# Performance work log

Measured on AMD Instinct MI355X. Metric: run time of the kernel, lower is better.

The kernel has to match this reference:

```python
import jax, jax.numpy as jnp
import numpy as np


def setup_inputs() -> dict:
    key = jax.random.key(0)
    k1, k2, k3 = jax.random.split(key, 3)
    B, C, H, W = 4, 320, 135, 240
    pnum = int(540 * 960 * 0.025)  # 12960, from shape=(540,960), sparse_rate=0.025
    x = jax.random.normal(k1, (B, C, H, W), dtype=jnp.float32)
    unc = jax.random.uniform(k2, (H, W), dtype=jnp.float32)
    prompts = jax.random.normal(k3, (pnum, C, 1, 1), dtype=jnp.float32)
    return {"x": x, "unc": unc, "prompts": prompts}


def reference(x, unc, prompts):
    # x: (B, C=320, H, W) bottleneck feature map; unc: (H, W); prompts: (pnum, C, 1, 1)
    H, W = x.shape[2], x.shape[3]
    pnum = prompts.shape[0]
    # descending top-k over flattened uncertainty map (== argsort()[::-1][:pnum])
    _, topk = jax.lax.top_k(unc.reshape(-1), pnum)  # (pnum,)
    hs = topk // W
    ws = topk % W
    # bilinear interpolation of a 1x1 spatial map is a pure broadcast, so
    # resized_prompt[j, :, 0, 0] == prompts[j, :, 0, 0]
    pv = prompts[:, :, 0, 0]  # (pnum, C)
    # scatter-add prompt vector j into feat[:, :, hs[j], ws[j]] across batch
    return x.at[:, :, hs, ws].add(pv.T[None])  # (B, C, H, W)
```

## Files before the change

### kernel.cpp

```cpp
#include <hip/hip_runtime.h>
#include <stdint.h>

#define BB    4
#define CC    320
#define HH    135
#define WW    240
#define HW    (HH*WW)
#define PNUM  12960
#define NBUCK 16384
#define MAXPER 32
#define P4    (HW/4)
#define NCH   4
#define NTILE ((CC/NCH)*P4)

typedef float f4 __attribute__((ext_vector_type(4)));
typedef unsigned u4 __attribute__((ext_vector_type(4)));

__global__ __launch_bounds__(256) void k_bucket(const float* __restrict__ unc,
                                                unsigned* __restrict__ hist,
                                                unsigned* __restrict__ members) {
    int i = blockIdx.x * 256 + threadIdx.x;
    if (i >= HW) return;
    float v = unc[i];
    int b = (int)(v * (float)NBUCK);
    b = b < 0 ? 0 : (b > NBUCK - 1 ? NBUCK - 1 : b);
    unsigned pos = atomicAdd(&hist[b], 1u);
    if (pos < MAXPER) members[(unsigned)b * MAXPER + pos] = (unsigned)i;
}

__global__ __launch_bounds__(1024) void k_scan(const unsigned* __restrict__ hist,
                                               unsigned* __restrict__ base) {
    __shared__ unsigned sh[1024];
    const int CH = NBUCK / 1024;
    int t = threadIdx.x;
    unsigned loc[CH];
    unsigned s = 0;
    #pragma unroll
    for (int k = 0; k < CH; ++k) { loc[k] = hist[t * CH + k]; s += loc[k]; }
    sh[t] = s;
    __syncthreads();
    for (int off = 1; off < 1024; off <<= 1) {
        unsigned v = (t + off < 1024) ? sh[t + off] : 0u;
        __syncthreads();
        sh[t] += v;
        __syncthreads();
    }
    unsigned run = sh[t] - s;
    #pragma unroll
    for (int k = CH - 1; k >= 0; --k) { base[t * CH + k] = run; run += loc[k]; }
}

__global__ __launch_bounds__(256) void k_rank(const float* __restrict__ unc,
                                              const unsigned* __restrict__ hist,
                                              const unsigned* __restrict__ base,
                                              const unsigned* __restrict__ members,
                                              unsigned* __restrict__ rank) {
    int i = blockIdx.x * 256 + threadIdx.x;
    if (i >= HW) return;
    float vi = unc[i];
    int b = (int)(vi * (float)NBUCK);
    b = b < 0 ? 0 : (b > NBUCK - 1 ? NBUCK - 1 : b);
    unsigned cnt = hist[b];
    if (cnt > MAXPER) cnt = MAXPER;
    unsigned r = base[b];
    for (unsigned k = 0; k < cnt; ++k) {
        unsigned j = members[(unsigned)b * MAXPER + k];
        if (j == (unsigned)i) continue;
        float vj = unc[j];
        r += (vj > vi) || (vj == vi && j < (unsigned)i);
    }
    rank[i] = r;
}

__global__ __launch_bounds__(256) void k_apply(const float* __restrict__ x,
                                               const float* __restrict__ prompts,
                                               const unsigned* __restrict__ rank,
                                               float* __restrict__ out) {
    int t = blockIdx.x * 256 + threadIdx.x;
    if (t >= NTILE) return;
    int cg = t / P4;
    int p4 = t - cg * P4;
    int c0 = cg * NCH;
    int p  = p4 * 4;

    u4 r4 = *(const u4*)(rank + p);

    float g[4][NCH];
    #pragma unroll
    for (int k = 0; k < 4; ++k) {
        unsigned r = r4[k];
        f4 gv = (f4)(0.0f);
        if (r < PNUM) gv = *(const f4*)(prompts + (size_t)r * CC + c0);
        #pragma unroll
        for (int j = 0; j < NCH; ++j) g[k][j] = gv[j];
    }

    #pragma unroll
    for (int b = 0; b < BB; ++b) {
        #pragma unroll
        for (int j = 0; j < NCH; ++j) {
            int off = (b * CC + c0 + j) * HW + p;
            f4 xv = __builtin_nontemporal_load((const f4*)(x + off));
            xv[0] += g[0][j]; xv[1] += g[1][j]; xv[2] += g[2][j]; xv[3] += g[3][j];
            __builtin_nontemporal_store(xv, (f4*)(out + off));
        }
    }
}

extern "C" void kernel_launch(void* const* d_in, const int* in_sizes, int n_in,
                              void* d_out, int out_size, void* d_ws, size_t ws_size,
                              hipStream_t stream) {
    const float* x       = (const float*)d_in[0];
    const float* unc     = (const float*)d_in[1];
    const float* prompts = (const float*)d_in[2];
    float* out = (float*)d_out;

    char* ws = (char*)d_ws;
    unsigned* hist    = (unsigned*)(ws);
    unsigned* base    = (unsigned*)(ws + (size_t)NBUCK * 4);
    unsigned* members = (unsigned*)(ws + (size_t)NBUCK * 8);
    unsigned* rank    = (unsigned*)(ws + (size_t)NBUCK * 8 + (size_t)NBUCK * MAXPER * 4);

    hipMemsetAsync(hist, 0, (size_t)NBUCK * 4, stream);
    k_bucket<<<(HW + 255) / 256, 256, 0, stream>>>(unc, hist, members);
    k_scan<<<1, 1024, 0, stream>>>(hist, base);
    k_rank<<<(HW + 255) / 256, 256, 0, stream>>>(unc, hist, base, members, rank);
    k_apply<<<(NTILE + 255) / 256, 256, 0, stream>>>(x, prompts, rank, out);
}
```

Before: 88.80 us.

## Precompute dense bf16 prompt-delta buffer and apply with contiguous loads

Adds a gather pass that writes a dense per-pixel, per-channel-group delta buffer in bf16, so the apply kernel reads contiguous vectors instead of doing random prompt gathers per tile. It also replaces hipMemsetAsync with a small zeroing kernel and drops the nontemporal load and store hints in the new apply path. The cost is an extra kernel launch and roughly 20 MB of extra memory traffic, and the bf16 rounding of the prompt values adds numerical error. The fallback path runs only when the workspace is too small.

Result: slower. 106.1 us (+19.4%).

```diff
diff --git a/kernel.cpp b/kernel.cpp
--- a/kernel.cpp
+++ b/kernel.cpp
@@ -11,10 +11,21 @@
 #define MAXPER 32
 #define P4    (HW/4)
 #define NCH   4
-#define NTILE ((CC/NCH)*P4)
+#define NCG   (CC/NCH)
+#define NTILE (NCG*P4)
 
 typedef float f4 __attribute__((ext_vector_type(4)));
 typedef unsigned u4 __attribute__((ext_vector_type(4)));
+
+__device__ inline unsigned short f2bf(float x) {
+    unsigned u = __float_as_uint(x);
+    return (unsigned short)((u + 0x7fffu + ((u >> 16) & 1u)) >> 16);
+}
+
+__global__ __launch_bounds__(256) void k_zero(unsigned* __restrict__ hist) {
+    int i = blockIdx.x * 256 + threadIdx.x;
+    if (i < NBUCK) hist[i] = 0u;
+}
 
 __global__ __launch_bounds__(256) void k_bucket(const float* __restrict__ unc,
                                                 unsigned* __restrict__ hist,
@@ -72,10 +83,25 @@
     rank[i] = r;
 }
 
-__global__ __launch_bounds__(256) void k_apply(const float* __restrict__ x,
-                                               const float* __restrict__ prompts,
-                                               const unsigned* __restrict__ rank,
-                                               float* __restrict__ out) {
+__global__ __launch_bounds__(256) void k_gather(const float* __restrict__ prompts,
+                                                const unsigned* __restrict__ rank,
+                                                unsigned* __restrict__ dbuf) {
+    int t = blockIdx.x * 256 + threadIdx.x;
+    if (t >= NCG * HW) return;
+    int cg = t / HW;
+    int p  = t - cg * HW;
+    unsigned r = rank[p];
+    f4 gv = (f4)(0.0f);
+    if (r < PNUM) gv = *(const f4*)(prompts + (size_t)r * CC + cg * 4);
+    uint2 w;
+    w.x = (unsigned)f2bf(gv[0]) | ((unsigned)f2bf(gv[1]) << 16);
+    w.y = (unsigned)f2bf(gv[2]) | ((unsigned)f2bf(gv[3]) << 16);
+    *(uint2*)(dbuf + 2 * (size_t)t) = w;
+}
+
+__global__ __launch_bounds__(256) void k_apply2(const float* __restrict__ x,
+                                                const unsigned* __restrict__ dbuf,
+                                                float* __restrict__ out) {
     int t = blockIdx.x * 256 + threadIdx.x;
     if (t >= NTILE) return;
     int cg = t / P4;
@@ -83,8 +109,45 @@
     int c0 = cg * NCH;
     int p  = p4 * 4;
 
+    const unsigned* dp = dbuf + 2 * ((size_t)cg * HW + p);
+    u4 A  = *(const u4*)dp;
+    u4 Bv = *(const u4*)(dp + 4);
+
+    float g[4][4];
+    #pragma unroll
+    for (int k = 0; k < 4; ++k) {
+        unsigned w0 = (k < 2) ? A[2 * k]     : Bv[2 * k - 4];
+        unsigned w1 = (k < 2) ? A[2 * k + 1] : Bv[2 * k - 3];
+        g[k][0] = __uint_as_float(w0 << 16);
+        g[k][1] = __uint_as_float(w0 & 0xffff0000u);
+        g[k][2] = __uint_as_float(w1 << 16);
+        g[k][3] = __uint_as_float(w1 & 0xffff0000u);
+    }
+
+    #pragma unroll
+    for (int b = 0; b < BB; ++b) {
+        #pragma unroll
+        for (int j = 0; j < NCH; ++j) {
+            int off = (b * CC + c0 + j) * HW + p;
+            f4 xv = *(const f4*)(x + off);
+            xv[0] += g[0][j]; xv[1] += g[1][j]; xv[2] += g[2][j]; xv[3] += g[3][j];
+            *(f4*)(out + off) = xv;
+        }
+    }
+}
+
+#define OFFS(it) ((((it) >> 2) * CC + c0 + ((it) & 3)) * HW + p)
+__global__ __launch_bounds__(256) void k_apply1(const float* __restrict__ x,
+                                                const float* __restrict__ prompts,
+                                                const unsigned* __restrict__ rank,
+                                                float* __restrict__ out) {
+    int t = blockIdx.x * 256 + threadIdx.x;
+    if (t >= NTILE) return;
+    int cg = t / P4;
+    int p4 = t - cg * P4;
+    int c0 = cg * NCH;
+    int p  = p4 * 4;
     u4 r4 = *(const u4*)(rank + p);
-
     float g[4][NCH];
     #pragma unroll
     for (int k = 0; k < 4; ++k) {
@@ -94,7 +157,6 @@
         #pragma unroll
         for (int j = 0; j < NCH; ++j) g[k][j] = gv[j];
     }
-
     #pragma unroll
     for (int b = 0; b < BB; ++b) {
         #pragma unroll
@@ -117,13 +179,21 @@
 
     char* ws = (char*)d_ws;
     unsigned* hist    = (unsigned*)(ws);
-    unsigned* base    = (unsigned*)(ws + (size_t)NBUCK * 4);
-    unsigned* members = (unsigned*)(ws + (size_t)NBUCK * 8);
-    unsigned* rank    = (unsigned*)(ws + (size_t)NBUCK * 8 + (size_t)NBUCK * MAXPER * 4);
+    unsigned* base    = (unsigned*)(ws + 65536);
+    unsigned* members = (unsigned*)(ws + 131072);
+    unsigned* rank    = (unsigned*)(ws + 131072 + 2097152);
+    unsigned* dbuf    = (unsigned*)(ws + 131072 + 2097152 + 129792);
+    const size_t need = 131072 + 2097152 + 129792 + (size_t)NCG * HW * 8;
 
-    hipMemsetAsync(hist, 0, (size_t)NBUCK * 4, stream);
+    k_zero<<<NBUCK / 256, 256, 0, stream>>>(hist);
     k_bucket<<<(HW + 255) / 256, 256, 0, stream>>>(unc, hist, members);
     k_scan<<<1, 1024, 0, stream>>>(hist, base);
     k_rank<<<(HW + 255) / 256, 256, 0, stream>>>(unc, hist, base, members, rank);
-    k_apply<<<(NTILE + 255) / 256, 256, 0, stream>>>(x, prompts, rank, out);
+
+    if (ws_size >= need) {
+        k_gather<<<(NCG * HW) / 256, 256, 0, stream>>>(prompts, rank, dbuf);
+        k_apply2<<<(NTILE + 255) / 256, 256, 0, stream>>>(x, dbuf, out);
+    } else {
+        k_apply1<<<(NTILE + 255) / 256, 256, 0, stream>>>(x, prompts, rank, out);
+    }
 }
```

## Precompute dense bf16 prompt delta map and stream-add it per batch slice

Applied to the files above, without the earlier changes.

Splits the apply step in two. A gather kernel first writes a dense per-channel delta map (the gathered prompts, rounded to bf16) into workspace. A simple 2D-grid kernel then adds that map to every (batch, channel) slice of x with coalesced vector loads and stores. The aim is to take the irregular prompt gather out of the main streaming pass. In exchange it adds an extra pass writing a roughly 20 MB buffer, loses precision by rounding prompt values to bf16, and drops the nontemporal hints. It also replaces hipMemsetAsync with a small zeroing kernel, and falls back to the old path if the workspace is too small.

Measured after the change: 104.7 us. +17.9%, slower.

```diff
diff --git a/kernel.cpp b/kernel.cpp
--- a/kernel.cpp
+++ b/kernel.cpp
@@ -11,10 +11,23 @@
 #define MAXPER 32
 #define P4    (HW/4)
 #define NCH   4
-#define NTILE ((CC/NCH)*P4)
+#define NCG   (CC/NCH)
+#define NTILE (NCG*P4)
+#define OCT   (HW/8)
 
 typedef float f4 __attribute__((ext_vector_type(4)));
 typedef unsigned u4 __attribute__((ext_vector_type(4)));
+typedef unsigned short us8 __attribute__((ext_vector_type(8)));
+
+__device__ inline unsigned short f2bf(float x) {
+    unsigned u = __float_as_uint(x);
+    return (unsigned short)((u + 0x7fffu + ((u >> 16) & 1u)) >> 16);
+}
+
+__global__ __launch_bounds__(256) void k_zero(unsigned* __restrict__ hist) {
+    int i = blockIdx.x * 256 + threadIdx.x;
+    if (i < NBUCK) hist[i] = 0u;
+}
 
 __global__ __launch_bounds__(256) void k_bucket(const float* __restrict__ unc,
                                                 unsigned* __restrict__ hist,
@@ -72,19 +85,65 @@
     rank[i] = r;
 }
 
-__global__ __launch_bounds__(256) void k_apply(const float* __restrict__ x,
-                                               const float* __restrict__ prompts,
-                                               const unsigned* __restrict__ rank,
-                                               float* __restrict__ out) {
+__global__ __launch_bounds__(256) void k_gather(const float* __restrict__ prompts,
+                                                const unsigned* __restrict__ rank,
+                                                unsigned short* __restrict__ dbufp) {
+    int t = blockIdx.x * 256 + threadIdx.x;
+    if (t >= NCG * OCT) return;
+    int cg = t / OCT;
+    int o8 = t - cg * OCT;
+    int p0 = o8 * 8;
+
+    u4 ra = *(const u4*)(rank + p0);
+    u4 rb = *(const u4*)(rank + p0 + 4);
+
+    unsigned short w[NCH][8];
+    #pragma unroll
+    for (int k = 0; k < 8; ++k) {
+        unsigned r = (k < 4) ? ra[k] : rb[k - 4];
+        f4 gv = (f4)(0.0f);
+        if (r < PNUM) gv = *(const f4*)(prompts + (size_t)r * CC + cg * 4);
+        #pragma unroll
+        for (int j = 0; j < NCH; ++j) w[j][k] = f2bf(gv[j]);
+    }
+    #pragma unroll
+    for (int j = 0; j < NCH; ++j) {
+        us8 v;
+        #pragma unroll
+        for (int k = 0; k < 8; ++k) v[k] = w[j][k];
+        *(us8*)(dbufp + (size_t)(cg * NCH + j) * HW + p0) = v;
+    }
+}
+
+__global__ __launch_bounds__(256) void k_apply3(const float* __restrict__ x,
+                                                const unsigned short* __restrict__ dbufp,
+                                                float* __restrict__ out) {
+    int p4 = blockIdx.x * 256 + threadIdx.x;
+    if (p4 >= P4) return;
+    int slice = blockIdx.y;
+    int c = slice % CC;
+    size_t off = (size_t)slice * HW + 4 * (size_t)p4;
+
+    uint2 d = *(const uint2*)(dbufp + (size_t)c * HW + 4 * p4);
+    f4 xv = *(const f4*)(x + off);
+    xv[0] += __uint_as_float(d.x << 16);
+    xv[1] += __uint_as_float(d.x & 0xffff0000u);
+    xv[2] += __uint_as_float(d.y << 16);
+    xv[3] += __uint_as_float(d.y & 0xffff0000u);
+    *(f4*)(out + off) = xv;
+}
+
+__global__ __launch_bounds__(256) void k_apply1(const float* __restrict__ x,
+                                                const float* __restrict__ prompts,
+                                                const unsigned* __restrict__ rank,
+                                                float* __restrict__ out) {
     int t = blockIdx.x * 256 + threadIdx.x;
     if (t >= NTILE) return;
     int cg = t / P4;
     int p4 = t - cg * P4;
     int c0 = cg * NCH;
     int p  = p4 * 4;
-
     u4 r4 = *(const u4*)(rank + p);
-
     float g[4][NCH];
     #pragma unroll
     for (int k = 0; k < 4; ++k) {
@@ -94,7 +153,6 @@
         #pragma unroll
         for (int j = 0; j < NCH; ++j) g[k][j] = gv[j];
     }
-
     #pragma unroll
     for (int b = 0; b < BB; ++b) {
         #pragma unroll
@@ -116,14 +174,23 @@
     float* out = (float*)d_out;
 
     char* ws = (char*)d_ws;
-    unsigned* hist    = (unsigned*)(ws);
-    unsigned* base    = (unsigned*)(ws + (size_t)NBUCK * 4);
-    unsigned* members = (unsigned*)(ws + (size_t)NBUCK * 8);
-    unsigned* rank    = (unsigned*)(ws + (size_t)NBUCK * 8 + (size_t)NBUCK * MAXPER * 4);
+    unsigned* hist         = (unsigned*)(ws);
+    unsigned* base         = (unsigned*)(ws + 65536);
+    unsigned* members      = (unsigned*)(ws + 131072);
+    unsigned* rank         = (unsigned*)(ws + 131072 + 2097152);
+    unsigned short* dbufp  = (unsigned short*)(ws + 131072 + 2097152 + 131072);
+    const size_t need = 131072 + 2097152 + 131072 + (size_t)CC * HW * 2;
 
-    hipMemsetAsync(hist, 0, (size_t)NBUCK * 4, stream);
+    k_zero<<<NBUCK / 256, 256, 0, stream>>>(hist);
     k_bucket<<<(HW + 255) / 256, 256, 0, stream>>>(unc, hist, members);
     k_scan<<<1, 1024, 0, stream>>>(hist, base);
     k_rank<<<(HW + 255) / 256, 256, 0, stream>>>(unc, hist, base, members, rank);
-    k_apply<<<(NTILE + 255) / 256, 256, 0, stream>>>(x, prompts, rank, out);
+
+    if (ws_size >= need) {
+        k_gather<<<(NCG * OCT + 255) / 256, 256, 0, stream>>>(prompts, rank, dbufp);
+        dim3 g((P4 + 255) / 256, BB * CC);
+        k_apply3<<<g, 256, 0, stream>>>(x, dbufp, out);
+    } else {
+        k_apply1<<<(NTILE + 255) / 256, 256, 0, stream>>>(x, prompts, rank, out);
+    }
 }
```
